# Optimization experiments

Measured on AMD Instinct MI355X. Metric: run time of the kernel, lower is better.

Reference implementation:

```python
import jax, jax.numpy as jnp
import numpy as np

C = 16          # scalar multiplicity of Rs_hidden = [(16, 0)]
NB = 10         # number_of_basis
H = 12          # radial MLP hidden size
MAX_R = 10.0
CENTERS = jnp.linspace(0.0, MAX_R, NB)
SIGMA = 0.8 * (MAX_R / (NB - 1))
GAUSS_NORM = 1.423085244900308   # e3nn GaussianRadialModel basis normalizer
Y0 = 1.0 / (2.0 * np.sqrt(np.pi))  # Y_{l=0} spherical harmonic constant


def setup_inputs() -> dict:
    key = jax.random.key(0)
    ks = jax.random.split(key, 9)
    z, n1, n2 = 4, 192, 192
    return {
        'input1': jax.random.normal(ks[0], (z, n1, C), jnp.float32),
        'input2': jax.random.normal(ks[1], (z, n2, C), jnp.float32),
        'xyz1': jax.random.normal(ks[2], (z, n1, 3), jnp.float32),
        'xyz2': jax.random.normal(ks[3], (z, n2, 3), jnp.float32),
        'mask': jax.random.randint(ks[4], (z, n1 + n2), 0, 2),
        'W_rad1': jax.random.normal(ks[5], (NB, H), jnp.float32),
        'W_rad_out': jax.random.normal(ks[6], (H, C * C), jnp.float32),
        'W_fc3': jax.random.normal(ks[7], (C, C), jnp.float32),
        'W_fc2': jax.random.normal(ks[8], (C, 1), jnp.float32),
    }


def _normalize(x, eps=1e-6):
    # torch .std defaults to unbiased (ddof=1)
    mean = x.mean(-1, keepdims=True)
    std = jnp.std(x, axis=-1, keepdims=True, ddof=1)
    return (x - mean) / (std + eps)


def reference(input1, input2, xyz1, xyz2, mask, W_rad1, W_rad_out, W_fc3, W_fc2):
    x = jnp.concatenate([input1, input2], axis=1)    # [z, n, C]
    xyz = jnp.concatenate([xyz1, xyz2], axis=1)      # [z, n, 3]
    z, n = x.shape[0], x.shape[1]

    # pairwise distances (eps keeps sqrt grad finite on the diagonal)
    diff = xyz[:, :, None, :] - xyz[:, None, :, :]   # [z, n, n, 3]
    d = jnp.sqrt(jnp.sum(diff * diff, axis=-1) + 1e-12)  # [z, n, n]

    # Gaussian radial basis + weight-normalized FC radial model (swish act)
    basis = jnp.exp(-jnp.square((d[..., None] - CENTERS) / SIGMA)) / GAUSS_NORM  # [z,n,n,NB]
    hmid = jax.nn.silu(basis @ W_rad1 / np.sqrt(NB))          # [z, n, n, H]
    R = hmid @ W_rad_out / np.sqrt(H)                         # [z, n, n, C*C]

    # l=0 TFN kernel: radial weights * Y_0 (trivial Clebsch-Gordan for scalars)
    K = R.reshape(z, n, n, C, C) * Y0                         # [z, a, b, i, j]
    y = jnp.einsum('zabij,zbj->zai', K, x)                    # [z, n, C]

    # Norm(Rs_hidden): per-irrep L2 norm; for scalars it's |x|
    y = jnp.abs(y)
    y = jnp.where(mask[..., None] == 0, 0.0, y)

    s = _normalize(jnp.sum(y, axis=1))                        # [z, C]
    h3 = jax.nn.leaky_relu(s @ W_fc3 / np.sqrt(C))            # fc3 + leaky_relu
    o = h3 @ W_fc2 / np.sqrt(C)                               # fc2
    return jax.nn.sigmoid(o).reshape(-1)                      # [z]
```

## Files before the change

kernel.cpp:

```cpp
#include <hip/hip_runtime.h>
#include <math.h>

#define Z     4
#define N1    192
#define NN    384
#define C     16
#define NB    10
#define H     12
#define ATILE 4
#define NAT   (NN / ATILE)
#define SPLIT 6

__device__ __forceinline__ float3 load_xyz(const float* __restrict__ xyz1,
                                           const float* __restrict__ xyz2,
                                           int z, int node) {
    const float* p = (node < N1) ? (xyz1 + (z * N1 + node) * 3)
                                 : (xyz2 + (z * N1 + (node - N1)) * 3);
    return make_float3(p[0], p[1], p[2]);
}

__global__ void k1_precompute_T(const float* __restrict__ in1,
                                const float* __restrict__ in2,
                                const float* __restrict__ Wro,
                                float* __restrict__ T) {
    const int bid = blockIdx.x;
    const int z = bid / NN, b = bid % NN;
    const int t = threadIdx.x;

    __shared__ float xl[C];
    if (t < C) {
        const float* xp = (b < N1) ? (in1 + (z * N1 + b) * C)
                                   : (in2 + (z * N1 + (b - N1)) * C);
        xl[t] = xp[t];
    }
    __syncthreads();

    const int h = t >> 4, i = t & 15;
    const float* w = Wro + h * (C * C) + i * C;
    float acc = 0.0f;
    #pragma unroll
    for (int j = 0; j < C; ++j) acc += w[j] * xl[j];

    const float scale = 0.28209479177387814f * 0.2886751345948129f;
    T[((z * H + h) * C + i) * NN + b] = acc * scale;
}

__global__ __launch_bounds__(128, 4) void k2_pairs(const float* __restrict__ xyz1,
                                                   const float* __restrict__ xyz2,
                                                   const float* __restrict__ Wr1,
                                                   const float* __restrict__ T,
                                                   float* __restrict__ partial) {
    const int bid = blockIdx.x;
    const int sp  = bid % SPLIT;
    const int za  = bid / SPLIT;
    const int z   = za / NAT, at = za % NAT;
    const int a0  = at * ATILE;
    const int tid = threadIdx.x;
    const int lane = tid & 63, wv = tid >> 6;
    const int b = sp * 64 + lane;

    __shared__ float W1s[NB * H];
    __shared__ float red[2][32];
    if (tid < NB * H)
        W1s[tid] = Wr1[tid] * (0.31622776601683794f * 0.7027283689263438f);
    __syncthreads();

    const float3 pb = load_xyz(xyz1, xyz2, z, b);
    const float invSigma = 1.125f;

    float dd[ATILE];
    #pragma unroll
    for (int aa = 0; aa < ATILE; ++aa) {
        const float3 pa = load_xyz(xyz1, xyz2, z, a0 + aa);
        const float dx = pa.x - pb.x, dy = pa.y - pb.y, dz = pa.z - pb.z;
        dd[aa] = sqrtf(dx * dx + dy * dy + dz * dz + 1e-12f);
    }

    float acc[ATILE][H];
    #pragma unroll
    for (int aa = 0; aa < ATILE; ++aa)
        #pragma unroll
        for (int h = 0; h < H; ++h) acc[aa][h] = 0.0f;

    #pragma unroll
    for (int k = 0; k < NB; ++k) {
        const float4 w0 = *(const float4*)&W1s[k * H + 0];
        const float4 w1 = *(const float4*)&W1s[k * H + 4];
        const float4 w2 = *(const float4*)&W1s[k * H + 8];
        const float ck = (float)k * (10.0f / 9.0f);
        #pragma unroll
        for (int aa = 0; aa < ATILE; ++aa) {
            const float u = (dd[aa] - ck) * invSigma;
            const float e = __expf(-u * u);
            acc[aa][0]  += e * w0.x;  acc[aa][1]  += e * w0.y;
            acc[aa][2]  += e * w0.z;  acc[aa][3]  += e * w0.w;
            acc[aa][4]  += e * w1.x;  acc[aa][5]  += e * w1.y;
            acc[aa][6]  += e * w1.z;  acc[aa][7]  += e * w1.w;
            acc[aa][8]  += e * w2.x;  acc[aa][9]  += e * w2.y;
            acc[aa][10] += e * w2.z;  acc[aa][11] += e * w2.w;
        }
    }
    float hm[ATILE][H];
    #pragma unroll
    for (int aa = 0; aa < ATILE; ++aa)
        #pragma unroll
        for (int h = 0; h < H; ++h)
            hm[aa][h] = acc[aa][h] / (1.0f + __expf(-acc[aa][h]));

    float v[ATILE * 8];
    #pragma unroll
    for (int p = 0; p < ATILE * 8; ++p) v[p] = 0.0f;

    const float* tb = T + ((z * H) * C + wv * 8) * NN + b;
    #pragma unroll
    for (int h = 0; h < H; ++h) {
        #pragma unroll
        for (int io = 0; io < 8; ++io) {
            const float tval = tb[(h * C + io) * NN];
            #pragma unroll
            for (int aa = 0; aa < ATILE; ++aa)
                v[aa * 8 + io] += hm[aa][h] * tval;
        }
    }

    #pragma unroll
    for (int k = 0; k < 5; ++k) {
        const int m = 16 >> k;
        const int bsel = (lane >> k) & 1;
        #pragma unroll
        for (int j = 0; j < m; ++j) {
            const float lo = v[j], hi = v[m + j];
            const float sendv = bsel ? lo : hi;
            const float recv = __shfl_xor(sendv, 1 << k, 64);
            v[j] = (bsel ? hi : lo) + recv;
        }
    }
    {
        const float recv = __shfl_xor(v[0], 32, 64);
        v[0] += recv;
    }
    const int l = lane & 31;
    const int pos = ((l & 1) << 4) | ((l & 2) << 2) | (l & 4) |
                    ((l & 8) >> 2) | ((l & 16) >> 4);
    if (lane < 32) red[wv][pos] = v[0];
    __syncthreads();

    if (tid < 64) {
        const int a_off = tid >> 4, i = tid & 15;
        const float val = (i < 8) ? red[0][a_off * 8 + i]
                                  : red[1][a_off * 8 + (i - 8)];
        partial[bid * 64 + tid] = val;
    }
}

__global__ __launch_bounds__(256) void k3_head(const float* __restrict__ partial,
                                               const int* __restrict__ mask,
                                               const float* __restrict__ Wfc3,
                                               const float* __restrict__ Wfc2,
                                               float* __restrict__ out) {
    const int z = blockIdx.x;
    const int t = threadIdx.x;
    const int i = t & 15, ch = t >> 4;

    __shared__ float red[16][17];
    __shared__ float sv[C];

    float acc = 0.0f;
    #pragma unroll
    for (int r = 0; r < 24; ++r) {
        const int a  = ch * 24 + r;
        const int at = a >> 2, t2 = a & 3;
        const int base = ((z * NAT + at) * SPLIT) * 64 + t2 * 16 + i;
        float val = 0.0f;
        #pragma unroll
        for (int s = 0; s < SPLIT; ++s) val += partial[base + s * 64];
        val = fabsf(val);
        if (mask[z * NN + a] != 0) acc += val;
    }
    red[ch][i] = acc;
    __syncthreads();
    if (t < C) {
        float s = 0.0f;
        #pragma unroll
        for (int c2 = 0; c2 < 16; ++c2) s += red[c2][t];
        sv[t] = s;
    }
    __syncthreads();

    if (t == 0) {
        float v[C];
        float mean = 0.0f;
        #pragma unroll
        for (int q = 0; q < C; ++q) { v[q] = sv[q]; mean += v[q]; }
        mean *= (1.0f / C);
        float var = 0.0f;
        #pragma unroll
        for (int q = 0; q < C; ++q) { const float d = v[q] - mean; var += d * d; }
        const float sd = sqrtf(var / (float)(C - 1)) + 1e-6f;
        #pragma unroll
        for (int q = 0; q < C; ++q) v[q] = (v[q] - mean) / sd;

        float o = 0.0f;
        #pragma unroll
        for (int k = 0; k < C; ++k) {
            float h3 = 0.0f;
            #pragma unroll
            for (int q = 0; q < C; ++q) h3 += v[q] * Wfc3[q * C + k];
            h3 *= 0.25f;
            h3 = (h3 > 0.0f) ? h3 : 0.01f * h3;
            o += h3 * Wfc2[k];
        }
        o *= 0.25f;
        out[z] = 1.0f / (1.0f + __expf(-o));
    }
}

extern "C" void kernel_launch(void* const* d_in, const int* in_sizes, int n_in,
                              void* d_out, int out_size, void* d_ws, size_t ws_size,
                              hipStream_t stream) {
    const float* in1  = (const float*)d_in[0];
    const float* in2  = (const float*)d_in[1];
    const float* xyz1 = (const float*)d_in[2];
    const float* xyz2 = (const float*)d_in[3];
    const int*   mask = (const int*)d_in[4];
    const float* Wr1  = (const float*)d_in[5];
    const float* Wro  = (const float*)d_in[6];
    const float* Wfc3 = (const float*)d_in[7];
    const float* Wfc2 = (const float*)d_in[8];
    float* out = (float*)d_out;

    float* T       = (float*)d_ws;
    float* partial = T + Z * NN * H * C;

    k1_precompute_T<<<Z * NN, 192, 0, stream>>>(in1, in2, Wro, T);
    k2_pairs<<<Z * NAT * SPLIT, 128, 0, stream>>>(xyz1, xyz2, Wr1, T, partial);
    k3_head<<<Z, 256, 0, stream>>>(partial, mask, Wfc3, Wfc2, out);
}
```

Measured before the change: 100.2 us.

## Use single-wave pair blocks with atomic accumulation and hardware exp/rcp

The pair kernel now runs one 64-lane wave per block that handles all 16 channels. This removes the shared-memory cross-wave reduction and its barrier. Per-block partials are replaced by atomicAdd into a y accumulator that the first kernel zeroes, so the head kernel reads one value per node instead of summing six splits. Exp and sigmoid use raw v_exp_f32/v_rcp_f32 inline asm, and the head's normalization and MLP are parallelized across 16 lanes with shuffles. The costs are twice as many registers per thread for the accumulators, atomic contention on 64 addresses per tile, and a non-deterministic summation order.

Result: faster. 95.45 us (-4.7%).

```diff
diff --git a/kernel.cpp b/kernel.cpp
--- a/kernel.cpp
+++ b/kernel.cpp
@@ -11,6 +11,13 @@
 #define NAT   (NN / ATILE)
 #define SPLIT 6
 
+__device__ __forceinline__ float fexp2(float x) {
+    float r; asm volatile("v_exp_f32 %0, %1" : "=v"(r) : "v"(x)); return r;
+}
+__device__ __forceinline__ float frcp(float x) {
+    float r; asm volatile("v_rcp_f32 %0, %1" : "=v"(r) : "v"(x)); return r;
+}
+
 __device__ __forceinline__ float3 load_xyz(const float* __restrict__ xyz1,
                                            const float* __restrict__ xyz2,
                                            int z, int node) {
@@ -22,7 +29,8 @@
 __global__ void k1_precompute_T(const float* __restrict__ in1,
                                 const float* __restrict__ in2,
                                 const float* __restrict__ Wro,
-                                float* __restrict__ T) {
+                                float* __restrict__ T,
+                                float* __restrict__ y_acc) {
     const int bid = blockIdx.x;
     const int z = bid / NN, b = bid % NN;
     const int t = threadIdx.x;
@@ -33,6 +41,7 @@
                                    : (in2 + (z * N1 + (b - N1)) * C);
         xl[t] = xp[t];
     }
+    if (bid < 128) y_acc[bid * 192 + t] = 0.0f;
     __syncthreads();
 
     const int h = t >> 4, i = t & 15;
@@ -45,28 +54,25 @@
     T[((z * H + h) * C + i) * NN + b] = acc * scale;
 }
 
-__global__ __launch_bounds__(128, 4) void k2_pairs(const float* __restrict__ xyz1,
-                                                   const float* __restrict__ xyz2,
-                                                   const float* __restrict__ Wr1,
-                                                   const float* __restrict__ T,
-                                                   float* __restrict__ partial) {
+__global__ __launch_bounds__(64) void k2_pairs(const float* __restrict__ xyz1,
+                                               const float* __restrict__ xyz2,
+                                               const float* __restrict__ Wr1,
+                                               const float* __restrict__ T,
+                                               float* __restrict__ y_acc) {
     const int bid = blockIdx.x;
     const int sp  = bid % SPLIT;
     const int za  = bid / SPLIT;
     const int z   = za / NAT, at = za % NAT;
     const int a0  = at * ATILE;
-    const int tid = threadIdx.x;
-    const int lane = tid & 63, wv = tid >> 6;
+    const int lane = threadIdx.x;
     const int b = sp * 64 + lane;
 
     __shared__ float W1s[NB * H];
-    __shared__ float red[2][32];
-    if (tid < NB * H)
-        W1s[tid] = Wr1[tid] * (0.31622776601683794f * 0.7027283689263438f);
+    for (int idx = lane; idx < NB * H; idx += 64)
+        W1s[idx] = Wr1[idx] * (0.31622776601683794f * 0.7027283689263438f);
     __syncthreads();
 
     const float3 pb = load_xyz(xyz1, xyz2, z, b);
-    const float invSigma = 1.125f;
 
     float dd[ATILE];
     #pragma unroll
@@ -76,11 +82,11 @@
         dd[aa] = sqrtf(dx * dx + dy * dy + dz * dz + 1e-12f);
     }
 
-    float acc[ATILE][H];
+    float hm[ATILE][H];
     #pragma unroll
     for (int aa = 0; aa < ATILE; ++aa)
         #pragma unroll
-        for (int h = 0; h < H; ++h) acc[aa][h] = 0.0f;
+        for (int h = 0; h < H; ++h) hm[aa][h] = 0.0f;
 
     #pragma unroll
     for (int k = 0; k < NB; ++k) {
@@ -90,42 +96,44 @@
         const float ck = (float)k * (10.0f / 9.0f);
         #pragma unroll
         for (int aa = 0; aa < ATILE; ++aa) {
-            const float u = (dd[aa] - ck) * invSigma;
-            const float e = __expf(-u * u);
-            acc[aa][0]  += e * w0.x;  acc[aa][1]  += e * w0.y;
-            acc[aa][2]  += e * w0.z;  acc[aa][3]  += e * w0.w;
-            acc[aa][4]  += e * w1.x;  acc[aa][5]  += e * w1.y;
-            acc[aa][6]  += e * w1.z;  acc[aa][7]  += e * w1.w;
-            acc[aa][8]  += e * w2.x;  acc[aa][9]  += e * w2.y;
-            acc[aa][10] += e * w2.z;  acc[aa][11] += e * w2.w;
-        }
-    }
-    float hm[ATILE][H];
+            const float t = dd[aa] - ck;
+            const float e = fexp2(t * t * -1.8259109111250943f);
+            hm[aa][0]  += e * w0.x;  hm[aa][1]  += e * w0.y;
+            hm[aa][2]  += e * w0.z;  hm[aa][3]  += e * w0.w;
+            hm[aa][4]  += e * w1.x;  hm[aa][5]  += e * w1.y;
+            hm[aa][6]  += e * w1.z;  hm[aa][7]  += e * w1.w;
+            hm[aa][8]  += e * w2.x;  hm[aa][9]  += e * w2.y;
+            hm[aa][10] += e * w2.z;  hm[aa][11] += e * w2.w;
+        }
+    }
     #pragma unroll
     for (int aa = 0; aa < ATILE; ++aa)
         #pragma unroll
-        for (int h = 0; h < H; ++h)
-            hm[aa][h] = acc[aa][h] / (1.0f + __expf(-acc[aa][h]));
-
-    float v[ATILE * 8];
-    #pragma unroll
-    for (int p = 0; p < ATILE * 8; ++p) v[p] = 0.0f;
-
-    const float* tb = T + ((z * H) * C + wv * 8) * NN + b;
+        for (int h = 0; h < H; ++h) {
+            const float x = hm[aa][h];
+            const float sig = frcp(1.0f + fexp2(x * -1.4426950408889634f));
+            hm[aa][h] = x * sig;
+        }
+
+    float v[ATILE * C];
+    #pragma unroll
+    for (int p = 0; p < ATILE * C; ++p) v[p] = 0.0f;
+
+    const float* tb = T + (z * H * C) * NN + b;
     #pragma unroll
     for (int h = 0; h < H; ++h) {
         #pragma unroll
-        for (int io = 0; io < 8; ++io) {
-            const float tval = tb[(h * C + io) * NN];
+        for (int i = 0; i < C; ++i) {
+            const float tval = tb[(h * C + i) * NN];
             #pragma unroll
             for (int aa = 0; aa < ATILE; ++aa)
-                v[aa * 8 + io] += hm[aa][h] * tval;
-        }
-    }
-
-    #pragma unroll
-    for (int k = 0; k < 5; ++k) {
-        const int m = 16 >> k;
+                v[aa * C + i] += hm[aa][h] * tval;
+        }
+    }
+
+    #pragma unroll
+    for (int k = 0; k < 6; ++k) {
+        const int m = 32 >> k;
         const int bsel = (lane >> k) & 1;
         #pragma unroll
         for (int j = 0; j < m; ++j) {
@@ -135,25 +143,13 @@
             v[j] = (bsel ? hi : lo) + recv;
         }
     }
-    {
-        const float recv = __shfl_xor(v[0], 32, 64);
-        v[0] += recv;
-    }
-    const int l = lane & 31;
-    const int pos = ((l & 1) << 4) | ((l & 2) << 2) | (l & 4) |
-                    ((l & 8) >> 2) | ((l & 16) >> 4);
-    if (lane < 32) red[wv][pos] = v[0];
-    __syncthreads();
-
-    if (tid < 64) {
-        const int a_off = tid >> 4, i = tid & 15;
-        const float val = (i < 8) ? red[0][a_off * 8 + i]
-                                  : red[1][a_off * 8 + (i - 8)];
-        partial[bid * 64 + tid] = val;
-    }
-}
-
-__global__ __launch_bounds__(256) void k3_head(const float* __restrict__ partial,
+    const int l = lane;
+    const int pos = ((l & 1) << 5) | ((l & 2) << 3) | ((l & 4) << 1) |
+                    ((l & 8) >> 1) | ((l & 16) >> 3) | ((l & 32) >> 5);
+    atomicAdd(&y_acc[(z * NN + a0) * C + pos], v[0]);
+}
+
+__global__ __launch_bounds__(256) void k3_head(const float* __restrict__ y_acc,
                                                const int* __restrict__ mask,
                                                const float* __restrict__ Wfc3,
                                                const float* __restrict__ Wfc2,
@@ -163,55 +159,44 @@
     const int i = t & 15, ch = t >> 4;
 
     __shared__ float red[16][17];
-    __shared__ float sv[C];
 
     float acc = 0.0f;
     #pragma unroll
     for (int r = 0; r < 24; ++r) {
-        const int a  = ch * 24 + r;
-        const int at = a >> 2, t2 = a & 3;
-        const int base = ((z * NAT + at) * SPLIT) * 64 + t2 * 16 + i;
-        float val = 0.0f;
-        #pragma unroll
-        for (int s = 0; s < SPLIT; ++s) val += partial[base + s * 64];
-        val = fabsf(val);
-        if (mask[z * NN + a] != 0) acc += val;
+        const int a = ch * 24 + r;
+        const float val = y_acc[(z * NN + a) * C + i];
+        if (mask[z * NN + a] != 0) acc += fabsf(val);
     }
     red[ch][i] = acc;
     __syncthreads();
+
     if (t < C) {
-        float s = 0.0f;
-        #pragma unroll
-        for (int c2 = 0; c2 < 16; ++c2) s += red[c2][t];
-        sv[t] = s;
-    }
-    __syncthreads();
-
-    if (t == 0) {
-        float v[C];
-        float mean = 0.0f;
-        #pragma unroll
-        for (int q = 0; q < C; ++q) { v[q] = sv[q]; mean += v[q]; }
-        mean *= (1.0f / C);
-        float var = 0.0f;
-        #pragma unroll
-        for (int q = 0; q < C; ++q) { const float d = v[q] - mean; var += d * d; }
-        const float sd = sqrtf(var / (float)(C - 1)) + 1e-6f;
-        #pragma unroll
-        for (int q = 0; q < C; ++q) v[q] = (v[q] - mean) / sd;
-
-        float o = 0.0f;
-        #pragma unroll
-        for (int k = 0; k < C; ++k) {
-            float h3 = 0.0f;
-            #pragma unroll
-            for (int q = 0; q < C; ++q) h3 += v[q] * Wfc3[q * C + k];
-            h3 *= 0.25f;
-            h3 = (h3 > 0.0f) ? h3 : 0.01f * h3;
-            o += h3 * Wfc2[k];
-        }
-        o *= 0.25f;
-        out[z] = 1.0f / (1.0f + __expf(-o));
+        float x = 0.0f;
+        #pragma unroll
+        for (int c2 = 0; c2 < 16; ++c2) x += red[c2][t];
+
+        float m = x;
+        #pragma unroll
+        for (int msk = 1; msk < 16; msk <<= 1) m += __shfl_xor(m, msk, 64);
+        m *= (1.0f / 16.0f);
+        const float dv = x - m;
+        float vv = dv * dv;
+        #pragma unroll
+        for (int msk = 1; msk < 16; msk <<= 1) vv += __shfl_xor(vv, msk, 64);
+        const float sd = sqrtf(vv / 15.0f) + 1e-6f;
+        const float xn = dv / sd;
+
+        float h3 = 0.0f;
+        #pragma unroll
+        for (int q = 0; q < 16; ++q)
+            h3 += __shfl(xn, q, 64) * Wfc3[q * C + t];
+        h3 *= 0.25f;
+        h3 = (h3 > 0.0f) ? h3 : 0.01f * h3;
+
+        float o = h3 * Wfc2[t];
+        #pragma unroll
+        for (int msk = 1; msk < 16; msk <<= 1) o += __shfl_xor(o, msk, 64);
+        if (t == 0) out[z] = 1.0f / (1.0f + __expf(-0.25f * o));
     }
 }
 
@@ -229,10 +214,10 @@
     const float* Wfc2 = (const float*)d_in[8];
     float* out = (float*)d_out;
 
-    float* T       = (float*)d_ws;
-    float* partial = T + Z * NN * H * C;
-
-    k1_precompute_T<<<Z * NN, 192, 0, stream>>>(in1, in2, Wro, T);
-    k2_pairs<<<Z * NAT * SPLIT, 128, 0, stream>>>(xyz1, xyz2, Wr1, T, partial);
-    k3_head<<<Z, 256, 0, stream>>>(partial, mask, Wfc3, Wfc2, out);
-}
+    float* T     = (float*)d_ws;
+    float* y_acc = T + Z * NN * H * C;
+
+    k1_precompute_T<<<Z * NN, 192, 0, stream>>>(in1, in2, Wro, T, y_acc);
+    k2_pairs<<<Z * NAT * SPLIT, 64, 0, stream>>>(xyz1, xyz2, Wr1, T, y_acc);
+    k3_head<<<Z, 256, 0, stream>>>(y_acc, mask, Wfc3, Wfc2, out);
+}
```
